# Performance work log

Hardware: AMD Instinct MI355X
Metric: run time of the kernel (lower is better)

## Reference

```python
import jax, jax.numpy as jnp
import numpy as np

N_RAYS = 1048576
N_SAMPLES = 64
FAR_DELTA = 1e10  # sentinel delta appended after last sample
EPS = 1e-10


def setup_inputs() -> dict:
    key = jax.random.key(0)
    k1, k2, k3 = jax.random.split(key, 3)
    sigmas = jax.random.normal(k1, (N_RAYS, N_SAMPLES), dtype=jnp.float32)
    rgbs = jax.random.uniform(k2, (N_RAYS, N_SAMPLES, 3), dtype=jnp.float32)
    # monotonically increasing z_vals per ray (near=2.0, positive strata)
    steps = jax.random.uniform(k3, (N_RAYS, N_SAMPLES), dtype=jnp.float32) * 0.05 + 0.01
    z_vals = 2.0 + jnp.cumsum(steps, axis=-1)
    return {"sigmas": sigmas, "rgbs": rgbs, "z_vals": z_vals}


def reference(sigmas, rgbs, z_vals):
    # deltas: (N, S); last delta is a huge value (opaque background)
    deltas = z_vals[:, 1:] - z_vals[:, :-1]
    deltas = jnp.concatenate(
        [deltas, jnp.full_like(deltas[:, :1], FAR_DELTA)], axis=-1)
    alphas = 1.0 - jnp.exp(-jax.nn.relu(sigmas) * deltas)          # (N, S)
    trans = 1.0 - alphas + EPS
    transmittance = jnp.concatenate(
        [jnp.ones_like(trans[:, :1]), trans], axis=-1)
    accum_trans = jnp.cumprod(transmittance, axis=-1)[:, :-1]       # (N, S)
    weights = alphas * accum_trans                                   # (N, S)
    rgb_final = jnp.sum(weights[..., None] * rgbs, axis=-2)          # (N, 3)
    depth_final = jnp.sum(weights * z_vals, axis=-1)                 # (N,)
    # white background compositing
    pix_alpha = jnp.sum(weights, axis=-1)                            # (N,)
    rgb_final = rgb_final + 1.0 - pix_alpha[:, None]
    return rgb_final, depth_final, accum_trans[:, -1]
```

## Files before the change

kernel.cpp:

```cpp
#include <hip/hip_runtime.h>

#define FARD 1e10f
#define EPSV 1e-10f

__global__ __launch_bounds__(256) void nerf_render_kernel(
    const float* __restrict__ sigmas,
    const float* __restrict__ rgbs,
    const float* __restrict__ z_vals,
    float* __restrict__ out,
    int n_rays)
{
    const int tid = blockIdx.x * blockDim.x + threadIdx.x;
    const int ray = tid >> 3;
    if (ray >= n_rays) return;
    const int l = threadIdx.x & 7;

    const float4* sp = reinterpret_cast<const float4*>(sigmas + (size_t)ray * 64 + l * 8);
    const float4* zp = reinterpret_cast<const float4*>(z_vals + (size_t)ray * 64 + l * 8);
    const float4* cp = reinterpret_cast<const float4*>(rgbs   + (size_t)ray * 192 + l * 24);
    const float4 s0 = sp[0], s1 = sp[1];
    const float4 z0 = zp[0], z1 = zp[1];
    const float4 c0 = cp[0], c1 = cp[1], c2 = cp[2];
    const float4 c3 = cp[3], c4 = cp[4], c5 = cp[5];

    const float zz[8] = {z0.x, z0.y, z0.z, z0.w, z1.x, z1.y, z1.z, z1.w};
    const float sv[8] = {s0.x, s0.y, s0.z, s0.w, s1.x, s1.y, s1.z, s1.w};
    const float cc[24] = {c0.x, c0.y, c0.z, c0.w, c1.x, c1.y, c1.z, c1.w,
                          c2.x, c2.y, c2.z, c2.w, c3.x, c3.y, c3.z, c3.w,
                          c4.x, c4.y, c4.z, c4.w, c5.x, c5.y, c5.z, c5.w};

    const float zn = __shfl_down(z0.x, 1, 8);

    float d[8];
    #pragma unroll
    for (int k = 0; k < 7; ++k) d[k] = zz[k + 1] - zz[k];
    d[7] = (l == 7) ? FARD : (zn - zz[7]);

    float run = 1.f;
    float P6  = 1.f;
    float Wp = 0.f, Dp = 0.f, Rp = 0.f, Gp = 0.f, Bp = 0.f;
    #pragma unroll
    for (int k = 0; k < 8; ++k) {
        const float e = __expf(-fmaxf(sv[k], 0.f) * d[k]);
        const float u = (1.f - e) * run;
        if (k == 7) P6 = run;
        run *= (e + EPSV);
        Wp += u;
        Dp += u * zz[k];
        Rp += u * cc[3 * k + 0];
        Gp += u * cc[3 * k + 1];
        Bp += u * cc[3 * k + 2];
    }

    float scan = run;
    #pragma unroll
    for (int off = 1; off < 8; off <<= 1) {
        const float v = __shfl_up(scan, off, 8);
        if (l >= off) scan *= v;
    }
    float ex = __shfl_up(scan, 1, 8);
    if (l == 0) ex = 1.f;

    float wsum = ex * Wp;
    float dsum = ex * Dp;
    float rsum = ex * Rp;
    float gsum = ex * Gp;
    float bsum = ex * Bp;
    #pragma unroll
    for (int off = 4; off >= 1; off >>= 1) {
        wsum += __shfl_xor(wsum, off, 8);
        dsum += __shfl_xor(dsum, off, 8);
        rsum += __shfl_xor(rsum, off, 8);
        gsum += __shfl_xor(gsum, off, 8);
        bsum += __shfl_xor(bsum, off, 8);
    }

    const float bg = 1.f - wsum;
    if (l < 3) {
        const float v = (l == 0) ? rsum : ((l == 1) ? gsum : bsum);
        out[(size_t)ray * 3 + l] = v + bg;
    } else if (l == 3) {
        out[(size_t)3 * n_rays + ray] = dsum;
    } else if (l == 7) {
        out[(size_t)4 * n_rays + ray] = ex * P6;
    }
}

extern "C" void kernel_launch(void* const* d_in, const int* in_sizes, int n_in,
                              void* d_out, int out_size, void* d_ws, size_t ws_size,
                              hipStream_t stream) {
    const float* sigmas = (const float*)d_in[0];
    const float* rgbs   = (const float*)d_in[1];
    const float* z_vals = (const float*)d_in[2];
    float* out = (float*)d_out;

    const int n_rays = in_sizes[0] / 64;
    const int threads = 256;
    const long long total_threads = (long long)n_rays * 8;
    const int blocks = (int)((total_threads + threads - 1) / threads);

    nerf_render_kernel<<<blocks, threads, 0, stream>>>(sigmas, rgbs, z_vals, out, n_rays);
}
```

Before: 240.8 us.

## Use persistent grid-stride loop with double-buffered ray loads

Replaces the one-ray-per-8-threads launch with a fixed grid of 2048 blocks that loops over rays in grid-stride order. The next ray's data is prefetched into a second register buffer while the current ray is processed, so load latency overlaps with compute. This keeps two rays' worth of inputs live per thread, raising register pressure and possibly lowering occupancy, and the fixed grid size may not match the machine's CU count well.

```diff
diff --git a/kernel.cpp b/kernel.cpp
--- a/kernel.cpp
+++ b/kernel.cpp
@@ -3,41 +3,46 @@
 #define FARD 1e10f
 #define EPSV 1e-10f
 
-__global__ __launch_bounds__(256) void nerf_render_kernel(
-    const float* __restrict__ sigmas,
-    const float* __restrict__ rgbs,
-    const float* __restrict__ z_vals,
-    float* __restrict__ out,
-    int n_rays)
-{
-    const int tid = blockIdx.x * blockDim.x + threadIdx.x;
-    const int ray = tid >> 3;
-    if (ray >= n_rays) return;
-    const int l = threadIdx.x & 7;
+struct RayData {
+    float4 s0, s1, z0, z1, c0, c1, c2, c3, c4, c5;
+};
 
+__device__ __forceinline__ void loadRay(RayData& r,
+                                        const float* __restrict__ sigmas,
+                                        const float* __restrict__ rgbs,
+                                        const float* __restrict__ z_vals,
+                                        int ray, int l) {
     const float4* sp = reinterpret_cast<const float4*>(sigmas + (size_t)ray * 64 + l * 8);
     const float4* zp = reinterpret_cast<const float4*>(z_vals + (size_t)ray * 64 + l * 8);
     const float4* cp = reinterpret_cast<const float4*>(rgbs   + (size_t)ray * 192 + l * 24);
-    const float4 s0 = sp[0], s1 = sp[1];
-    const float4 z0 = zp[0], z1 = zp[1];
-    const float4 c0 = cp[0], c1 = cp[1], c2 = cp[2];
-    const float4 c3 = cp[3], c4 = cp[4], c5 = cp[5];
+    r.s0 = sp[0]; r.s1 = sp[1];
+    r.z0 = zp[0]; r.z1 = zp[1];
+    r.c0 = cp[0]; r.c1 = cp[1]; r.c2 = cp[2];
+    r.c3 = cp[3]; r.c4 = cp[4]; r.c5 = cp[5];
+}
 
-    const float zz[8] = {z0.x, z0.y, z0.z, z0.w, z1.x, z1.y, z1.z, z1.w};
-    const float sv[8] = {s0.x, s0.y, s0.z, s0.w, s1.x, s1.y, s1.z, s1.w};
-    const float cc[24] = {c0.x, c0.y, c0.z, c0.w, c1.x, c1.y, c1.z, c1.w,
-                          c2.x, c2.y, c2.z, c2.w, c3.x, c3.y, c3.z, c3.w,
-                          c4.x, c4.y, c4.z, c4.w, c5.x, c5.y, c5.z, c5.w};
+__device__ __forceinline__ void processRay(const RayData& rd,
+                                           float* __restrict__ out,
+                                           int ray, int l, int n_rays) {
+    const float zz[8] = {rd.z0.x, rd.z0.y, rd.z0.z, rd.z0.w,
+                         rd.z1.x, rd.z1.y, rd.z1.z, rd.z1.w};
+    const float sv[8] = {rd.s0.x, rd.s0.y, rd.s0.z, rd.s0.w,
+                         rd.s1.x, rd.s1.y, rd.s1.z, rd.s1.w};
+    const float cc[24] = {rd.c0.x, rd.c0.y, rd.c0.z, rd.c0.w,
+                          rd.c1.x, rd.c1.y, rd.c1.z, rd.c1.w,
+                          rd.c2.x, rd.c2.y, rd.c2.z, rd.c2.w,
+                          rd.c3.x, rd.c3.y, rd.c3.z, rd.c3.w,
+                          rd.c4.x, rd.c4.y, rd.c4.z, rd.c4.w,
+                          rd.c5.x, rd.c5.y, rd.c5.z, rd.c5.w};
 
-    const float zn = __shfl_down(z0.x, 1, 8);
+    const float zn = __shfl_down(rd.z0.x, 1, 8);
 
     float d[8];
     #pragma unroll
     for (int k = 0; k < 7; ++k) d[k] = zz[k + 1] - zz[k];
     d[7] = (l == 7) ? FARD : (zn - zz[7]);
 
-    float run = 1.f;
-    float P6  = 1.f;
+    float run = 1.f, P6 = 1.f;
     float Wp = 0.f, Dp = 0.f, Rp = 0.f, Gp = 0.f, Bp = 0.f;
     #pragma unroll
     for (int k = 0; k < 8; ++k) {
@@ -61,11 +66,8 @@
     float ex = __shfl_up(scan, 1, 8);
     if (l == 0) ex = 1.f;
 
-    float wsum = ex * Wp;
-    float dsum = ex * Dp;
-    float rsum = ex * Rp;
-    float gsum = ex * Gp;
-    float bsum = ex * Bp;
+    float wsum = ex * Wp, dsum = ex * Dp;
+    float rsum = ex * Rp, gsum = ex * Gp, bsum = ex * Bp;
     #pragma unroll
     for (int off = 4; off >= 1; off >>= 1) {
         wsum += __shfl_xor(wsum, off, 8);
@@ -86,6 +88,40 @@
     }
 }
 
+__global__ __launch_bounds__(256) void nerf_render_kernel(
+    const float* __restrict__ sigmas,
+    const float* __restrict__ rgbs,
+    const float* __restrict__ z_vals,
+    float* __restrict__ out,
+    int n_rays)
+{
+    const int l = threadIdx.x & 7;
+    const int T = gridDim.x * blockDim.x;
+    const int nseg = n_rays * 8;
+
+    int sA = blockIdx.x * blockDim.x + threadIdx.x;
+    if (sA >= nseg) return;
+
+    RayData A, B;
+    loadRay(A, sigmas, rgbs, z_vals, sA >> 3, l);
+    int sB = sA + T;
+
+    #pragma unroll 1
+    while (sB < nseg) {
+        loadRay(B, sigmas, rgbs, z_vals, sB >> 3, l);
+        processRay(A, out, sA >> 3, l, n_rays);
+        sA = sB + T;
+        if (sA >= nseg) {
+            processRay(B, out, sB >> 3, l, n_rays);
+            return;
+        }
+        loadRay(A, sigmas, rgbs, z_vals, sA >> 3, l);
+        processRay(B, out, sB >> 3, l, n_rays);
+        sB = sA + T;
+    }
+    processRay(A, out, sA >> 3, l, n_rays);
+}
+
 extern "C" void kernel_launch(void* const* d_in, const int* in_sizes, int n_in,
                               void* d_out, int out_size, void* d_ws, size_t ws_size,
                               hipStream_t stream) {
@@ -96,8 +132,7 @@
 
     const int n_rays = in_sizes[0] / 64;
     const int threads = 256;
-    const long long total_threads = (long long)n_rays * 8;
-    const int blocks = (int)((total_threads + threads - 1) / threads);
+    const int blocks = 2048;
 
     nerf_render_kernel<<<blocks, threads, 0, stream>>>(sigmas, rgbs, z_vals, out, n_rays);
 }
```

New measurement: 264.3 us. +9.8%, slower.
